# Kernel optimization log

Hardware: AMD Instinct MI355X
Metric: run time of the kernel (lower is better)

Reference implementation:

```python
import jax, jax.numpy as jnp
import numpy as np

H = 1024; NH = 16; HD = H // NH  # hidden, heads, head_dim

def setup_inputs() -> dict:
    key = jax.random.key(0)
    ks = jax.random.split(key, 9)
    s = 1.0 / np.sqrt(H)
    return {
        "hidden_states": jax.random.normal(ks[0], (2, 2048, H), jnp.float32),
        "Wq": jax.random.uniform(ks[1], (H, H), jnp.float32, -s, s),
        "bq": jnp.zeros((H,), jnp.float32),
        "Wk": jax.random.uniform(ks[2], (H, H), jnp.float32, -s, s),
        "bk": jnp.zeros((H,), jnp.float32),
        "Wv": jax.random.uniform(ks[3], (H, H), jnp.float32, -s, s),
        "bv": jnp.zeros((H,), jnp.float32),
        "Wo": jax.random.uniform(ks[4], (H, H), jnp.float32, -s, s),
        "bo": jnp.zeros((H,), jnp.float32),
    }

def reference(hidden_states, Wq, bq, Wk, bk, Wv, bv, Wo, bo):
    B, S, _ = hidden_states.shape
    def heads(x):  # [B,S,H] -> [B,NH,S,HD]
        return x.reshape(B, S, NH, HD).transpose(0, 2, 1, 3)
    q = heads(hidden_states @ Wq + bq)
    k = heads(hidden_states @ Wk + bk)
    v = heads(hidden_states @ Wv + bv)
    scores = jnp.einsum('bhqd,bhkd->bhqk', q, k) / jnp.sqrt(jnp.float32(HD))
    causal = jnp.where(jnp.tril(jnp.ones((S, S), bool)), 0.0, -jnp.inf)
    probs = jax.nn.softmax(scores + causal[None, None], axis=-1)
    ctx = jnp.einsum('bhqk,bhkd->bhqd', probs, v)
    ctx = ctx.transpose(0, 2, 1, 3).reshape(B, S, H)
    return ctx @ Wo + bo
```

## Files before the change

kernel.cpp:

```cpp
#include <hip/hip_runtime.h>
#include <hip/hip_bf16.h>

#define BB 2
#define SS 2048
#define HH 1024
#define NHH 16
#define HDD 64
#define MM (BB*SS)
#define QKV_N (3*HH)

typedef _Float16 f16x8 __attribute__((ext_vector_type(8)));
typedef _Float16 f16x4 __attribute__((ext_vector_type(4)));
typedef float f32x4 __attribute__((ext_vector_type(4)));

#define MFMA16(a,b,c) __builtin_amdgcn_mfma_f32_16x16x32_f16((a),(b),(c),0,0,0)

__device__ __forceinline__ void gl2lds16(const _Float16* g, _Float16* l) {
    __builtin_amdgcn_global_load_lds(
        (const __attribute__((address_space(1))) void*)g,
        (__attribute__((address_space(3))) void*)l, 16, 0, 0);
}

__global__ void cast4_kernel(const float* __restrict__ x, _Float16* __restrict__ y, int n4) {
    int i = blockIdx.x * blockDim.x + threadIdx.x;
    if (i < n4) {
        float4 v = ((const float4*)x)[i];
        f16x4 h = {(_Float16)v.x, (_Float16)v.y, (_Float16)v.z, (_Float16)v.w};
        ((f16x4*)y)[i] = h;
    }
}

__global__ __launch_bounds__(256) void transpose_kernel(
    const float* __restrict__ W0, const float* __restrict__ W1,
    const float* __restrict__ W2, const float* __restrict__ W3,
    _Float16* __restrict__ WqkvT, _Float16* __restrict__ WoT)
{
    __shared__ float t[64][65];
    int z = blockIdx.z;
    const float* src = (z == 0) ? W0 : (z == 1) ? W1 : (z == 2) ? W2 : W3;
    _Float16* dst = (z < 3) ? (WqkvT + (size_t)z * HH * HH) : WoT;
    int k0 = blockIdx.y * 64, n0 = blockIdx.x * 64;
    int tid = threadIdx.x;

#pragma unroll
    for (int p = 0; p < 4; ++p) {
        int row = p * 16 + (tid >> 4);
        int col4 = (tid & 15) * 4;
        float4 v = *(const float4*)&src[(size_t)(k0 + row) * HH + n0 + col4];
        t[row][col4 + 0] = v.x; t[row][col4 + 1] = v.y;
        t[row][col4 + 2] = v.z; t[row][col4 + 3] = v.w;
    }
    __syncthreads();
#pragma unroll
    for (int p = 0; p < 2; ++p) {
        int nc = p * 32 + (tid >> 3);
        int ch = tid & 7;
        f16x8 o;
#pragma unroll
        for (int j = 0; j < 8; ++j) o[j] = (_Float16)t[ch * 8 + j][nc];
        *(f16x8*)&dst[(size_t)(n0 + nc) * HH + k0 + ch * 8] = o;
    }
}

template<int MODE>
__global__ __launch_bounds__(256) void gemm128_kernel(
    const _Float16* __restrict__ A, const _Float16* __restrict__ Bt,
    const float* __restrict__ bias0, const float* __restrict__ bias1, const float* __restrict__ bias2,
    _Float16* __restrict__ Qh, _Float16* __restrict__ Kh, _Float16* __restrict__ Vt,
    float* __restrict__ Out)
{
    const int K = HH;
    const int NT = K / 32;
    __shared__ _Float16 smem[24576];

    int row0 = blockIdx.y * 128, n0 = blockIdx.x * 128;
    int tid = threadIdx.x;
    int w = tid >> 6, l = tid & 63, m16 = l & 15, quad = l >> 4;
    int wm = w >> 1, wn = w & 1;

    int srow = w * 32 + (l >> 2);
    int sch = (l & 3) ^ ((l >> 2) & 3) ^ ((l >> 4) & 3);
    const _Float16* aptr = A + (size_t)(row0 + srow) * K + sch * 8;
    const _Float16* bptr = Bt + (size_t)(n0 + srow) * K + sch * 8;

    int gsw = (m16 & 3) ^ ((m16 >> 2) & 3);
    int acol = (quad ^ gsw) * 8;

    f32x4 zero4 = {0.f, 0.f, 0.f, 0.f};
    f32x4 acc[4][4];
#pragma unroll
    for (int i = 0; i < 4; ++i)
#pragma unroll
        for (int j = 0; j < 4; ++j) acc[i][j] = zero4;

    auto stage = [&](int t, int s) {
        int k0 = t * 32;
        int ao = s * 4096 + (w * 32) * 32;
        int bo = 12288 + s * 4096 + (w * 32) * 32;
        gl2lds16(aptr + k0, smem + ao);
        gl2lds16(aptr + (size_t)16 * K + k0, smem + ao + 16 * 32);
        gl2lds16(bptr + k0, smem + bo);
        gl2lds16(bptr + (size_t)16 * K + k0, smem + bo + 16 * 32);
    };

    stage(0, 0);
    stage(1, 1);
    int cur = 0;
    for (int t = 0; t < NT; ++t) {
        if (t < NT - 1) asm volatile("s_waitcnt vmcnt(4)" ::: "memory");
        else            asm volatile("s_waitcnt vmcnt(0)" ::: "memory");
        asm volatile("s_barrier" ::: "memory");
        if (t + 2 < NT) {
            int nxt = cur + 2; if (nxt >= 3) nxt -= 3;
            stage(t + 2, nxt);
        }
        const _Float16* Asr = smem + cur * 4096;
        const _Float16* Bsr = smem + 12288 + cur * 4096;
        f16x8 af[4], bf[4];
#pragma unroll
        for (int i = 0; i < 4; ++i)
            af[i] = *(const f16x8*)&Asr[(wm * 64 + i * 16 + m16) * 32 + acol];
#pragma unroll
        for (int j = 0; j < 4; ++j)
            bf[j] = *(const f16x8*)&Bsr[(wn * 64 + j * 16 + m16) * 32 + acol];
#pragma unroll
        for (int i = 0; i < 4; ++i)
#pragma unroll
            for (int j = 0; j < 4; ++j)
                acc[i][j] = MFMA16(af[i], bf[j], acc[i][j]);
        cur = (cur == 2) ? 0 : cur + 1;
    }

    if (MODE == 1) {
#pragma unroll
        for (int j = 0; j < 4; ++j) {
            int n = n0 + wn * 64 + j * 16 + m16;
            float bi = bias0[n];
#pragma unroll
            for (int i = 0; i < 4; ++i)
#pragma unroll
                for (int r = 0; r < 4; ++r) {
                    int mg = row0 + wm * 64 + i * 16 + quad * 4 + r;
                    Out[(size_t)mg * HH + n] = acc[i][j][r] + bi;
                }
        }
        return;
    }

    int which = n0 >> 10;
    const float* bias = (which == 0) ? bias0 : (which == 1) ? bias1 : bias2;
    __syncthreads();
#pragma unroll
    for (int j = 0; j < 4; ++j) {
        int n_local = wn * 64 + j * 16 + m16;
        float bi = bias[(n0 + n_local) & 1023];
#pragma unroll
        for (int i = 0; i < 4; ++i)
#pragma unroll
            for (int r = 0; r < 4; ++r) {
                int m_local = wm * 64 + i * 16 + quad * 4 + r;
                float v = acc[i][j][r] + bi;
                if (which == 0) v *= 0.18033688011112042f;
                if (which == 2) smem[n_local * 132 + m_local] = (_Float16)v;
                else            smem[m_local * 132 + n_local] = (_Float16)v;
            }
    }
    __syncthreads();

    int b = row0 >> 11, s0 = row0 & 2047;
    if (which == 2) {
#pragma unroll
        for (int p = 0; p < 8; ++p) {
            int n_local = p * 16 + (tid >> 4);
            int schunk = tid & 15;
            f16x8 v = *(const f16x8*)&smem[n_local * 132 + schunk * 8];
            int nw = (n0 + n_local) & 1023;
            int hh = nw >> 6, d = nw & 63;
            *(f16x8*)&Vt[((size_t)(b * NHH + hh) * HDD + d) * SS + s0 + schunk * 8] = v;
        }
    } else {
        _Float16* dst = (which == 0) ? Qh : Kh;
        int hh0 = (n0 & 1023) >> 6;
#pragma unroll
        for (int p = 0; p < 8; ++p) {
            int m_local = p * 16 + (tid >> 4);
            int seg = tid & 15;
            f16x8 v = *(const f16x8*)&smem[m_local * 132 + seg * 8];
            int hh = hh0 + (seg >> 3), d = (seg & 7) * 8;
            *(f16x8*)&dst[((size_t)(b * NHH + hh) * SS + s0 + m_local) * HDD + d] = v;
        }
    }
}

__global__ __launch_bounds__(256, 2) void attn_kernel(
    const _Float16* __restrict__ Qh, const _Float16* __restrict__ Kh,
    const _Float16* __restrict__ Vt, _Float16* __restrict__ Ctx)
{
    __shared__ _Float16 KV[3 * 8192];
    __shared__ _Float16 Pl[4][2][16][72];

    int tid = threadIdx.x;
    int w = tid >> 6, l = tid & 63;
    int m16 = l & 15, quad = l >> 4;
    int b = blockIdx.z, h = blockIdx.y;
    int tA = blockIdx.x, tB = 31 - tA;

    const _Float16* Q = Qh + (size_t)(b * NHH + h) * SS * HDD;
    const _Float16* K = Kh + (size_t)(b * NHH + h) * SS * HDD;
    const _Float16* V = Vt + (size_t)(b * NHH + h) * HDD * SS;

    int qbA = tA * 64 + w * 16, qbB = tB * 64 + w * 16;
    f16x8 aqA0 = *(const f16x8*)(Q + (size_t)(qbA + m16) * HDD + quad * 8);
    f16x8 aqA1 = *(const f16x8*)(Q + (size_t)(qbA + m16) * HDD + 32 + quad * 8);
    f16x8 aqB0 = *(const f16x8*)(Q + (size_t)(qbB + m16) * HDD + quad * 8);
    f16x8 aqB1 = *(const f16x8*)(Q + (size_t)(qbB + m16) * HDD + 32 + quad * 8);

    int srow = w * 16 + (l >> 3);
    int sch = (l & 7) ^ (l >> 3);
    const _Float16* kg = K + (size_t)srow * HDD + sch * 8;
    const _Float16* vg = V + (size_t)srow * SS + sch * 8;

    auto stage = [&](int t, int s) {
        int kt = t * 64;
        _Float16* kb = &KV[s * 8192];
        _Float16* vb = &KV[s * 8192 + 4096];
        gl2lds16(kg + (size_t)kt * HDD, kb + (w * 16) * 64);
        gl2lds16(kg + (size_t)(kt + 8) * HDD, kb + (w * 16 + 8) * 64);
        gl2lds16(vg + kt, vb + (w * 16) * 64);
        gl2lds16(vg + (size_t)8 * SS + kt, vb + (w * 16 + 8) * 64);
    };

    int swz = m16 & 7;
    int cka = (quad ^ swz) * 8;
    int ckb = ((quad + 4) ^ swz) * 8;

    f32x4 zero4 = {0.f, 0.f, 0.f, 0.f};
    f32x4 oA[4], oB[4];
#pragma unroll
    for (int c = 0; c < 4; ++c) { oA[c] = zero4; oB[c] = zero4; }
    float lsA[4] = {0.f, 0.f, 0.f, 0.f}, lsB[4] = {0.f, 0.f, 0.f, 0.f};

    stage(0, 0);
    if (1 <= tB) stage(1, 1);
    int cur = 0;
    for (int t = 0; t <= tB; ++t) {
        int kt = t * 64;
        bool doA = (t <= tA);
        if (t < tB) asm volatile("s_waitcnt vmcnt(4)" ::: "memory");
        else        asm volatile("s_waitcnt vmcnt(0)" ::: "memory");
        asm volatile("s_barrier" ::: "memory");
        if (t + 2 <= tB) {
            int nxt = cur + 2; if (nxt >= 3) nxt -= 3;
            stage(t + 2, nxt);
        }

        const _Float16* kb = &KV[cur * 8192];
        const _Float16* vb = &KV[cur * 8192 + 4096];
        f16x8 bk[4][2], bv[4][2];
#pragma unroll
        for (int s = 0; s < 4; ++s) {
            const _Float16* kr = kb + (s * 16 + m16) * 64;
            bk[s][0] = *(const f16x8*)(kr + cka);
            bk[s][1] = *(const f16x8*)(kr + ckb);
        }
#pragma unroll
        for (int c = 0; c < 4; ++c) {
            const _Float16* vr = vb + (c * 16 + m16) * 64;
            bv[c][0] = *(const f16x8*)(vr + cka);
            bv[c][1] = *(const f16x8*)(vr + ckb);
        }

        f32x4 scB[4], scA[4];
#pragma unroll
        for (int s = 0; s < 4; ++s) {
            scB[s] = MFMA16(aqB0, bk[s][0], zero4);
            scB[s] = MFMA16(aqB1, bk[s][1], scB[s]);
        }
        if (doA) {
#pragma unroll
            for (int s = 0; s < 4; ++s) {
                scA[s] = MFMA16(aqA0, bk[s][0], zero4);
                scA[s] = MFMA16(aqA1, bk[s][1], scA[s]);
            }
        }

#pragma unroll
        for (int s = 0; s < 4; ++s) {
            int key = kt + s * 16 + m16;
#pragma unroll
            for (int r = 0; r < 4; ++r) {
                int qrow = qbB + quad * 4 + r;
                float p = (key > qrow) ? 0.0f : exp2f(scB[s][r]);
                lsB[r] += p;
                Pl[w][0][quad * 4 + r][s * 16 + m16] = (_Float16)p;
            }
        }
        if (doA) {
#pragma unroll
            for (int s = 0; s < 4; ++s) {
                int key = kt + s * 16 + m16;
#pragma unroll
                for (int r = 0; r < 4; ++r) {
                    int qrow = qbA + quad * 4 + r;
                    float p = (key > qrow) ? 0.0f : exp2f(scA[s][r]);
                    lsA[r] += p;
                    Pl[w][1][quad * 4 + r][s * 16 + m16] = (_Float16)p;
                }
            }
        }
        asm volatile("s_waitcnt lgkmcnt(0)" ::: "memory");

        f16x8 pfB0 = *(const f16x8*)&Pl[w][0][m16][quad * 8];
        f16x8 pfB1 = *(const f16x8*)&Pl[w][0][m16][32 + quad * 8];
#pragma unroll
        for (int c = 0; c < 4; ++c) {
            oB[c] = MFMA16(pfB0, bv[c][0], oB[c]);
            oB[c] = MFMA16(pfB1, bv[c][1], oB[c]);
        }
        if (doA) {
            f16x8 pfA0 = *(const f16x8*)&Pl[w][1][m16][quad * 8];
            f16x8 pfA1 = *(const f16x8*)&Pl[w][1][m16][32 + quad * 8];
#pragma unroll
            for (int c = 0; c < 4; ++c) {
                oA[c] = MFMA16(pfA0, bv[c][0], oA[c]);
                oA[c] = MFMA16(pfA1, bv[c][1], oA[c]);
            }
        }
        cur = (cur == 2) ? 0 : cur + 1;
    }

#pragma unroll
    for (int half = 0; half < 2; ++half) {
        f32x4* o = half ? oB : oA;
        float* ls = half ? lsB : lsA;
        int qb = half ? qbB : qbA;
#pragma unroll
        for (int r = 0; r < 4; ++r) {
            float rs = ls[r];
#pragma unroll
            for (int off = 1; off < 16; off <<= 1) rs += __shfl_xor(rs, off);
            float inv = 1.0f / rs;
            size_t rowoff = ((size_t)(b * SS) + qb + quad * 4 + r) * HH + h * HDD;
#pragma unroll
            for (int c = 0; c < 4; ++c)
                Ctx[rowoff + c * 16 + m16] = (_Float16)(o[c][r] * inv);
        }
    }
}

extern "C" void kernel_launch(void* const* d_in, const int* in_sizes, int n_in,
                              void* d_out, int out_size, void* d_ws, size_t ws_size,
                              hipStream_t stream) {
    const float* hs = (const float*)d_in[0];
    const float* Wq = (const float*)d_in[1];
    const float* bq = (const float*)d_in[2];
    const float* Wk = (const float*)d_in[3];
    const float* bk = (const float*)d_in[4];
    const float* Wv = (const float*)d_in[5];
    const float* bv = (const float*)d_in[6];
    const float* Wo = (const float*)d_in[7];
    const float* bo = (const float*)d_in[8];
    float* out = (float*)d_out;

    size_t off = 0;
    auto alloc = [&](size_t bytes) {
        void* p = (char*)d_ws + off;
        off += (bytes + 255) & ~(size_t)255;
        return p;
    };
    _Float16* Xh    = (_Float16*)alloc((size_t)MM * HH * 2);
    _Float16* WqkvT = (_Float16*)alloc((size_t)3 * HH * HH * 2);
    _Float16* WoT   = (_Float16*)alloc((size_t)HH * HH * 2);
    _Float16* Qh    = (_Float16*)alloc((size_t)BB * NHH * SS * HDD * 2);
    _Float16* Kh    = (_Float16*)alloc((size_t)BB * NHH * SS * HDD * 2);
    _Float16* Vt    = (_Float16*)alloc((size_t)BB * NHH * SS * HDD * 2);
    _Float16* Ctx   = (_Float16*)alloc((size_t)MM * HH * 2);

    cast4_kernel<<<(MM * HH / 4 + 255) / 256, 256, 0, stream>>>(hs, Xh, MM * HH / 4);
    transpose_kernel<<<dim3(16, 16, 4), 256, 0, stream>>>(Wq, Wk, Wv, Wo, WqkvT, WoT);
    gemm128_kernel<0><<<dim3(QKV_N / 128, MM / 128), 256, 0, stream>>>(
        Xh, WqkvT, bq, bk, bv, Qh, Kh, Vt, nullptr);
    attn_kernel<<<dim3(16, NHH, BB), 256, 0, stream>>>(Qh, Kh, Vt, Ctx);
    gemm128_kernel<1><<<dim3(HH / 128, MM / 128), 256, 0, stream>>>(
        Ctx, WoT, bo, bo, bo, nullptr, nullptr, nullptr, out);
}
```

Baseline: 201.6 us.

## Compute transposed scores so P stays in registers, removing LDS round-trip

The attention kernel now computes S^T = K·Q^T, so each lane holds the probabilities for one query row across keys. Those values are packed directly as the B operand of 16x16x16 MFMAs computing O^T = V^T·P^T, which removes the shared-memory P buffer, its writes and reads, and the lgkmcnt wait. Row sums become per-lane scalars reduced with two shuffles, and the output is written as 4-wide f16 vectors. In exchange the PV step issues twice as many smaller-K MFMAs and V is read as 4-element chunks with a new swizzled offset.

```diff
diff --git a/kernel.cpp b/kernel.cpp
--- a/kernel.cpp
+++ b/kernel.cpp
@@ -13,7 +13,8 @@
 typedef _Float16 f16x4 __attribute__((ext_vector_type(4)));
 typedef float f32x4 __attribute__((ext_vector_type(4)));
 
-#define MFMA16(a,b,c) __builtin_amdgcn_mfma_f32_16x16x32_f16((a),(b),(c),0,0,0)
+#define MFMA16(a,b,c)  __builtin_amdgcn_mfma_f32_16x16x32_f16((a),(b),(c),0,0,0)
+#define MFMA16K16(a,b,c) __builtin_amdgcn_mfma_f32_16x16x16f16((a),(b),(c),0,0,0)
 
 __device__ __forceinline__ void gl2lds16(const _Float16* g, _Float16* l) {
     __builtin_amdgcn_global_load_lds(
@@ -197,7 +198,6 @@
     const _Float16* __restrict__ Vt, _Float16* __restrict__ Ctx)
 {
     __shared__ _Float16 KV[3 * 8192];
-    __shared__ _Float16 Pl[4][2][16][72];
 
     int tid = threadIdx.x;
     int w = tid >> 6, l = tid & 63;
@@ -210,10 +210,11 @@
     const _Float16* V = Vt + (size_t)(b * NHH + h) * HDD * SS;
 
     int qbA = tA * 64 + w * 16, qbB = tB * 64 + w * 16;
-    f16x8 aqA0 = *(const f16x8*)(Q + (size_t)(qbA + m16) * HDD + quad * 8);
-    f16x8 aqA1 = *(const f16x8*)(Q + (size_t)(qbA + m16) * HDD + 32 + quad * 8);
-    f16x8 aqB0 = *(const f16x8*)(Q + (size_t)(qbB + m16) * HDD + quad * 8);
-    f16x8 aqB1 = *(const f16x8*)(Q + (size_t)(qbB + m16) * HDD + 32 + quad * 8);
+    int qA = qbA + m16, qB = qbB + m16;
+    f16x8 aqA0 = *(const f16x8*)(Q + (size_t)qA * HDD + quad * 8);
+    f16x8 aqA1 = *(const f16x8*)(Q + (size_t)qA * HDD + 32 + quad * 8);
+    f16x8 aqB0 = *(const f16x8*)(Q + (size_t)qB * HDD + quad * 8);
+    f16x8 aqB1 = *(const f16x8*)(Q + (size_t)qB * HDD + 32 + quad * 8);
 
     int srow = w * 16 + (l >> 3);
     int sch = (l & 7) ^ (l >> 3);
@@ -233,12 +234,16 @@
     int swz = m16 & 7;
     int cka = (quad ^ swz) * 8;
     int ckb = ((quad + 4) ^ swz) * 8;
+    int vco[4];
+#pragma unroll
+    for (int s = 0; s < 4; ++s)
+        vco[s] = (((s * 2 + (quad >> 1)) ^ swz) * 8) + (quad & 1) * 4;
 
     f32x4 zero4 = {0.f, 0.f, 0.f, 0.f};
     f32x4 oA[4], oB[4];
 #pragma unroll
     for (int c = 0; c < 4; ++c) { oA[c] = zero4; oB[c] = zero4; }
-    float lsA[4] = {0.f, 0.f, 0.f, 0.f}, lsB[4] = {0.f, 0.f, 0.f, 0.f};
+    float lsA = 0.f, lsB = 0.f;
 
     stage(0, 0);
     if (1 <= tB) stage(1, 1);
@@ -256,75 +261,69 @@
 
         const _Float16* kb = &KV[cur * 8192];
         const _Float16* vb = &KV[cur * 8192 + 4096];
-        f16x8 bk[4][2], bv[4][2];
+        f16x8 bk[4][2];
 #pragma unroll
         for (int s = 0; s < 4; ++s) {
             const _Float16* kr = kb + (s * 16 + m16) * 64;
             bk[s][0] = *(const f16x8*)(kr + cka);
             bk[s][1] = *(const f16x8*)(kr + ckb);
         }
+        f16x4 av[4][4];
 #pragma unroll
         for (int c = 0; c < 4; ++c) {
             const _Float16* vr = vb + (c * 16 + m16) * 64;
-            bv[c][0] = *(const f16x8*)(vr + cka);
-            bv[c][1] = *(const f16x8*)(vr + ckb);
-        }
-
-        f32x4 scB[4], scA[4];
-#pragma unroll
-        for (int s = 0; s < 4; ++s) {
-            scB[s] = MFMA16(aqB0, bk[s][0], zero4);
-            scB[s] = MFMA16(aqB1, bk[s][1], scB[s]);
+#pragma unroll
+            for (int s = 0; s < 4; ++s)
+                av[c][s] = *(const f16x4*)(vr + vco[s]);
+        }
+
+        {
+            f32x4 st[4];
+#pragma unroll
+            for (int s = 0; s < 4; ++s) {
+                st[s] = MFMA16(bk[s][0], aqB0, zero4);
+                st[s] = MFMA16(bk[s][1], aqB1, st[s]);
+            }
+            f16x4 pt[4];
+#pragma unroll
+            for (int s = 0; s < 4; ++s) {
+#pragma unroll
+                for (int r = 0; r < 4; ++r) {
+                    int key = kt + s * 16 + quad * 4 + r;
+                    float p = (key > qB) ? 0.0f : exp2f(st[s][r]);
+                    lsB += p;
+                    pt[s][r] = (_Float16)p;
+                }
+            }
+#pragma unroll
+            for (int c = 0; c < 4; ++c)
+#pragma unroll
+                for (int s = 0; s < 4; ++s)
+                    oB[c] = MFMA16K16(av[c][s], pt[s], oB[c]);
         }
         if (doA) {
+            f32x4 st[4];
 #pragma unroll
             for (int s = 0; s < 4; ++s) {
-                scA[s] = MFMA16(aqA0, bk[s][0], zero4);
-                scA[s] = MFMA16(aqA1, bk[s][1], scA[s]);
-            }
-        }
-
-#pragma unroll
-        for (int s = 0; s < 4; ++s) {
-            int key = kt + s * 16 + m16;
-#pragma unroll
-            for (int r = 0; r < 4; ++r) {
-                int qrow = qbB + quad * 4 + r;
-                float p = (key > qrow) ? 0.0f : exp2f(scB[s][r]);
-                lsB[r] += p;
-                Pl[w][0][quad * 4 + r][s * 16 + m16] = (_Float16)p;
-            }
-        }
-        if (doA) {
+                st[s] = MFMA16(bk[s][0], aqA0, zero4);
+                st[s] = MFMA16(bk[s][1], aqA1, st[s]);
+            }
+            f16x4 pt[4];
 #pragma unroll
             for (int s = 0; s < 4; ++s) {
-                int key = kt + s * 16 + m16;
 #pragma unroll
                 for (int r = 0; r < 4; ++r) {
-                    int qrow = qbA + quad * 4 + r;
-                    float p = (key > qrow) ? 0.0f : exp2f(scA[s][r]);
-                    lsA[r] += p;
-                    Pl[w][1][quad * 4 + r][s * 16 + m16] = (_Float16)p;
+                    int key = kt + s * 16 + quad * 4 + r;
+                    float p = (key > qA) ? 0.0f : exp2f(st[s][r]);
+                    lsA += p;
+                    pt[s][r] = (_Float16)p;
                 }
             }
-        }
-        asm volatile("s_waitcnt lgkmcnt(0)" ::: "memory");
-
-        f16x8 pfB0 = *(const f16x8*)&Pl[w][0][m16][quad * 8];
-        f16x8 pfB1 = *(const f16x8*)&Pl[w][0][m16][32 + quad * 8];
-#pragma unroll
-        for (int c = 0; c < 4; ++c) {
-            oB[c] = MFMA16(pfB0, bv[c][0], oB[c]);
-            oB[c] = MFMA16(pfB1, bv[c][1], oB[c]);
-        }
-        if (doA) {
-            f16x8 pfA0 = *(const f16x8*)&Pl[w][1][m16][quad * 8];
-            f16x8 pfA1 = *(const f16x8*)&Pl[w][1][m16][32 + quad * 8];
-#pragma unroll
-            for (int c = 0; c < 4; ++c) {
-                oA[c] = MFMA16(pfA0, bv[c][0], oA[c]);
-                oA[c] = MFMA16(pfA1, bv[c][1], oA[c]);
-            }
+#pragma unroll
+            for (int c = 0; c < 4; ++c)
+#pragma unroll
+                for (int s = 0; s < 4; ++s)
+                    oA[c] = MFMA16K16(av[c][s], pt[s], oA[c]);
         }
         cur = (cur == 2) ? 0 : cur + 1;
     }
@@ -332,18 +331,19 @@
 #pragma unroll
     for (int half = 0; half < 2; ++half) {
         f32x4* o = half ? oB : oA;
-        float* ls = half ? lsB : lsA;
-        int qb = half ? qbB : qbA;
-#pragma unroll
-        for (int r = 0; r < 4; ++r) {
-            float rs = ls[r];
-#pragma unroll
-            for (int off = 1; off < 16; off <<= 1) rs += __shfl_xor(rs, off);
-            float inv = 1.0f / rs;
-            size_t rowoff = ((size_t)(b * SS) + qb + quad * 4 + r) * HH + h * HDD;
-#pragma unroll
-            for (int c = 0; c < 4; ++c)
-                Ctx[rowoff + c * 16 + m16] = (_Float16)(o[c][r] * inv);
+        float ls = half ? lsB : lsA;
+        int qg = half ? (qbB + m16) : (qbA + m16);
+        float rs = ls;
+        rs += __shfl_xor(rs, 16);
+        rs += __shfl_xor(rs, 32);
+        float inv = 1.0f / rs;
+        size_t rowoff = ((size_t)(b * SS) + qg) * HH + h * HDD;
+#pragma unroll
+        for (int c = 0; c < 4; ++c) {
+            f16x4 ov;
+#pragma unroll
+            for (int r = 0; r < 4; ++r) ov[r] = (_Float16)(o[c][r] * inv);
+            *(f16x4*)&Ctx[rowoff + c * 16 + quad * 4] = ov;
         }
     }
 }
```

New measurement: 195.6 us. 3.0% less time.
